# Kernel tuning notes

Hardware: AMD Instinct MI355X
Metric: run time of the kernel (lower is better)

## Reference

```python
import jax, jax.numpy as jnp
import numpy as np

N = 4096  # input_features == output_features == transform length (power of 2)


def _fft(x, twiddle_factors):
    """Faithful vectorized form of the module's radix-2 butterfly network.

    x: (N, D) complex64. twiddle_factors: (N, D) float32 (the learned weights).
    Original loop: for each stage `step`, for each block, for r in [0, half):
        k = r * (N // step)
        temp = exp(-2j*pi*k/N * twiddle_factors[k]) * x[j + half]
        new x[j + half] = x[j] - temp ; new x[j] = x[j] + temp
    Blocks are independent, so each stage is a single batched butterfly.
    """
    n = x.shape[0]
    # initial permutation: index xor with N//2 (as written in the source; not full bit-reversal)
    x = x[jnp.bitwise_xor(jnp.arange(n), n // 2)]
    step = 2
    while step <= n:  # log2(N) stages, fixed small Python loop
        half = step // 2
        k = jnp.arange(half) * (n // step)                      # (half,)
        phase = (-2.0 * jnp.pi) * (k[:, None].astype(jnp.float32) / n) * twiddle_factors[k]
        tw = jnp.exp(1j * phase)                                # (half, D) complex64
        xr = x.reshape(n // step, step, -1)                     # (blocks, step, D)
        top = xr[:, :half]
        bot = xr[:, half:]
        temp = tw[None] * bot                                   # (blocks, half, D)
        x = jnp.concatenate([top + temp, top - temp], axis=1).reshape(n, -1)
        step *= 2
    return x


def setup_inputs() -> dict:
    key = jax.random.key(0)
    kx, kw = jax.random.split(key)
    x = jax.random.normal(kx, (N, N), dtype=jnp.float32)
    weights = jax.random.normal(kw, (N, N), dtype=jnp.float32)  # nn.Parameter(randn(out, in))
    return {"x": x, "weights": weights}


def reference(x, weights):
    # input_features == output_features -> no pad / no truncation branch taken
    return _fft(x.astype(jnp.complex64), weights)
```

## Files before the change

kernel.cpp:

```cpp
#include <hip/hip_runtime.h>

#define FFT_N 4096
#define NEG_TWOPI -6.28318530717958647692f

__global__ __launch_bounds__(256) void fft_lo(const float* __restrict__ x,
                                              const float* __restrict__ w,
                                              float4* __restrict__ dst4,
                                              unsigned dst_lim4) {
    __shared__ __align__(16) float2 tile[64 * 64];
    const int t  = threadIdx.x;
    const int c0 = (blockIdx.x & 63) << 6;
    const int r0 = (blockIdx.x >> 6) << 6;
    const int src_r0 = r0 ^ 2048;

    const float4* x4    = (const float4*)x;
    float4*       tile4 = (float4*)tile;
#pragma unroll
    for (int l = 0; l < 4; ++l) {
        int idx = l * 256 + t;
        int row = idx >> 4;
        int cg  = idx & 15;
        float4 v = x4[(size_t)(src_r0 + row) * 1024 + (c0 >> 2) + cg];
        tile4[(row << 5) + (cg << 1) + 0] = make_float4(v.x, 0.f, v.y, 0.f);
        tile4[(row << 5) + (cg << 1) + 1] = make_float4(v.z, 0.f, v.w, 0.f);
    }
    __syncthreads();

    const int c  = t & 63;
    const int pb = t >> 6;
#pragma unroll
    for (int step = 2; step <= 64; step <<= 1) {
        const int half = step >> 1;
        const int kmul = FFT_N / step;
#pragma unroll
        for (int q = 0; q < 8; ++q) {
            const int p    = pb * 8 + q;
            const int blk  = p / half;
            const int r    = p - blk * half;
            const int itop = blk * step + r;
            const int k    = r * kmul;
            const float wk = w[(size_t)k * FFT_N + c0 + c];
            const float phase = NEG_TWOPI * ((float)k * (1.0f / 4096.0f)) * wk;
            float s, cs;
            __sincosf(phase, &s, &cs);
            float2 a = tile[(itop << 6) + c];
            float2 b = tile[((itop + half) << 6) + c];
            float tr = cs * b.x - s * b.y;
            float ti = cs * b.y + s * b.x;
            tile[(itop << 6) + c]          = make_float2(a.x + tr, a.y + ti);
            tile[((itop + half) << 6) + c] = make_float2(a.x - tr, a.y - ti);
        }
        __syncthreads();
    }

#pragma unroll
    for (int l = 0; l < 8; ++l) {
        int idx = l * 256 + t;
        int row = idx >> 5;
        int cp  = idx & 31;
        size_t gi = (size_t)(r0 + row) * 2048 + (c0 >> 1) + cp;
        if (gi < dst_lim4) dst4[gi] = tile4[(row << 5) + cp];
    }
}

template <int REAL_OUT>
__global__ __launch_bounds__(256) void fft_hi(const float* __restrict__ w,
                                              const float4* __restrict__ src4,
                                              float4* __restrict__ dst4,
                                              unsigned src_lim4,
                                              unsigned dst_lim4) {
    __shared__ __align__(16) float2 tile[64 * 64];
    const int t    = threadIdx.x;
    const int c0   = (blockIdx.x & 63) << 6;
    const int rres = blockIdx.x >> 6;

    float4* tile4 = (float4*)tile;
#pragma unroll
    for (int l = 0; l < 8; ++l) {
        int idx = l * 256 + t;
        int j   = idx >> 5;
        int cp  = idx & 31;
        size_t gi = (size_t)(rres + (j << 6)) * 2048 + (c0 >> 1) + cp;
        tile4[(j << 5) + cp] = (gi < src_lim4) ? src4[gi]
                                               : make_float4(0.f, 0.f, 0.f, 0.f);
    }
    __syncthreads();

    const int c  = t & 63;
    const int pb = t >> 6;
#pragma unroll
    for (int h = 1; h <= 32; h <<= 1) {
        const int kmul = 32 / h;
#pragma unroll
        for (int q = 0; q < 8; ++q) {
            const int p    = pb * 8 + q;
            const int blk  = p / h;
            const int r    = p - blk * h;
            const int jtop = blk * (h << 1) + r;
            const int k    = (rres + (r << 6)) * kmul;
            const float wk = w[(size_t)k * FFT_N + c0 + c];
            const float phase = NEG_TWOPI * ((float)k * (1.0f / 4096.0f)) * wk;
            float s, cs;
            __sincosf(phase, &s, &cs);
            float2 a = tile[(jtop << 6) + c];
            float2 b = tile[((jtop + h) << 6) + c];
            float tr = cs * b.x - s * b.y;
            float ti = cs * b.y + s * b.x;
            tile[(jtop << 6) + c]       = make_float2(a.x + tr, a.y + ti);
            tile[((jtop + h) << 6) + c] = make_float2(a.x - tr, a.y - ti);
        }
        __syncthreads();
    }

    if (REAL_OUT) {
#pragma unroll
        for (int l = 0; l < 4; ++l) {
            int idx = l * 256 + t;
            int j   = idx >> 4;
            int g   = idx & 15;
            float4 v;
            v.x = tile[(j << 6) + 4 * g + 0].x;
            v.y = tile[(j << 6) + 4 * g + 1].x;
            v.z = tile[(j << 6) + 4 * g + 2].x;
            v.w = tile[(j << 6) + 4 * g + 3].x;
            size_t gi = (size_t)(rres + (j << 6)) * 1024 + (c0 >> 2) + g;
            if (gi < dst_lim4) dst4[gi] = v;
        }
    } else {
#pragma unroll
        for (int l = 0; l < 8; ++l) {
            int idx = l * 256 + t;
            int j   = idx >> 5;
            int cp  = idx & 31;
            size_t gi = (size_t)(rres + (j << 6)) * 2048 + (c0 >> 1) + cp;
            if (gi < dst_lim4) dst4[gi] = tile4[(j << 5) + cp];
        }
    }
}

extern "C" void kernel_launch(void* const* d_in, const int* in_sizes, int n_in,
                              void* d_out, int out_size, void* d_ws, size_t ws_size,
                              hipStream_t stream) {
    const float* x = (const float*)d_in[0];
    const float* w = (const float*)d_in[1];
    const long long NN = (long long)FFT_N * FFT_N;

    if ((long long)out_size >= 2 * NN) {
        float4* o4 = (float4*)d_out;
        unsigned lim4 = (unsigned)(out_size / 4);
        fft_lo<<<4096, 256, 0, stream>>>(x, w, o4, lim4);
        fft_hi<0><<<4096, 256, 0, stream>>>(w, o4, o4, lim4, lim4);
    } else {
        float4* ws4 = (float4*)d_ws;
        unsigned ws_lim4  = (unsigned)(ws_size / 16);
        unsigned out_lim4 = (unsigned)(out_size / 4);
        fft_lo<<<4096, 256, 0, stream>>>(x, w, ws4, ws_lim4);
        fft_hi<1><<<4096, 256, 0, stream>>>(w, (const float4*)ws4, (float4*)d_out,
                                            ws_lim4, out_lim4);
    }
}
```

Measured before the change: 235.9 us.

## Do 64-point butterfly stages in registers with one shared-memory transpose

Each thread now keeps 16 complex values in registers. The first four butterfly stages run on those registers, then one shared-memory exchange regroups the data for the last two stages, in both the low and high FFT kernels. This replaces six shared-memory read/write rounds and barriers per kernel with two. It also reduces twiddle loads and sincos calls, because each twiddle is computed once per r and reused across blocks, and the r=0 twiddle is skipped in fft_lo. The cost is higher register pressure, with 32 floats per thread.

```diff
diff --git a/kernel.cpp b/kernel.cpp
--- a/kernel.cpp
+++ b/kernel.cpp
@@ -1,7 +1,14 @@
 #include <hip/hip_runtime.h>
 
-#define FFT_N 4096
 #define NEG_TWOPI -6.28318530717958647692f
+
+__device__ __forceinline__ void bf(float& ar, float& ai, float& br, float& bi,
+                                   float s, float cs) {
+    float tr = cs * br - s * bi;
+    float ti = cs * bi + s * br;
+    br = ar - tr; bi = ai - ti;
+    ar = ar + tr; ai = ai + ti;
+}
 
 __global__ __launch_bounds__(256) void fft_lo(const float* __restrict__ x,
                                               const float* __restrict__ w,
@@ -28,31 +35,71 @@
 
     const int c  = t & 63;
     const int pb = t >> 6;
-#pragma unroll
-    for (int step = 2; step <= 64; step <<= 1) {
-        const int half = step >> 1;
-        const int kmul = FFT_N / step;
-#pragma unroll
-        for (int q = 0; q < 8; ++q) {
-            const int p    = pb * 8 + q;
-            const int blk  = p / half;
-            const int r    = p - blk * half;
-            const int itop = blk * step + r;
-            const int k    = r * kmul;
-            const float wk = w[(size_t)k * FFT_N + c0 + c];
-            const float phase = NEG_TWOPI * ((float)k * (1.0f / 4096.0f)) * wk;
-            float s, cs;
-            __sincosf(phase, &s, &cs);
-            float2 a = tile[(itop << 6) + c];
-            float2 b = tile[((itop + half) << 6) + c];
-            float tr = cs * b.x - s * b.y;
-            float ti = cs * b.y + s * b.x;
-            tile[(itop << 6) + c]          = make_float2(a.x + tr, a.y + ti);
-            tile[((itop + half) << 6) + c] = make_float2(a.x - tr, a.y - ti);
-        }
-        __syncthreads();
-    }
-
+
+    float ar[16], ai[16];
+#pragma unroll
+    for (int m = 0; m < 16; ++m) {
+        float2 v = tile[(16 * pb + m) * 64 + c];
+        ar[m] = v.x; ai[m] = v.y;
+    }
+
+#pragma unroll
+    for (int h = 1; h <= 8; h <<= 1) {
+        const int step = h << 1;
+        const int kmul = 4096 / step;
+#pragma unroll
+        for (int r = 0; r < h; ++r) {
+            float s = 0.f, cs = 1.f;
+            if (r != 0) {
+                const int k = r * kmul;
+                const float wk = w[(size_t)k * 4096 + c0 + c];
+                __sincosf(NEG_TWOPI * ((float)k * (1.f / 4096.f)) * wk, &s, &cs);
+            }
+#pragma unroll
+            for (int b = 0; b < 8 / h; ++b) {
+                const int mt = b * step + r;
+                bf(ar[mt], ai[mt], ar[mt + h], ai[mt + h], s, cs);
+            }
+        }
+    }
+
+#pragma unroll
+    for (int m = 0; m < 16; ++m)
+        tile[(16 * pb + m) * 64 + c] = make_float2(ar[m], ai[m]);
+    __syncthreads();
+#pragma unroll
+    for (int m = 0; m < 16; ++m) {
+        float2 v = tile[(pb + 4 * m) * 64 + c];
+        ar[m] = v.x; ai[m] = v.y;
+    }
+
+#pragma unroll
+    for (int rm = 0; rm < 4; ++rm) {
+        const int j = pb + 4 * rm;
+        const int k = j * 128;
+        float s, cs;
+        const float wk = w[(size_t)k * 4096 + c0 + c];
+        __sincosf(NEG_TWOPI * ((float)k * (1.f / 4096.f)) * wk, &s, &cs);
+#pragma unroll
+        for (int b = 0; b < 2; ++b) {
+            const int mt = b * 8 + rm;
+            bf(ar[mt], ai[mt], ar[mt + 4], ai[mt + 4], s, cs);
+        }
+    }
+#pragma unroll
+    for (int m = 0; m < 8; ++m) {
+        const int j = pb + 4 * m;
+        const int k = j * 64;
+        float s, cs;
+        const float wk = w[(size_t)k * 4096 + c0 + c];
+        __sincosf(NEG_TWOPI * ((float)k * (1.f / 4096.f)) * wk, &s, &cs);
+        bf(ar[m], ai[m], ar[m + 8], ai[m + 8], s, cs);
+    }
+
+#pragma unroll
+    for (int m = 0; m < 16; ++m)
+        tile[(pb + 4 * m) * 64 + c] = make_float2(ar[m], ai[m]);
+    __syncthreads();
 #pragma unroll
     for (int l = 0; l < 8; ++l) {
         int idx = l * 256 + t;
@@ -88,29 +135,69 @@
 
     const int c  = t & 63;
     const int pb = t >> 6;
-#pragma unroll
-    for (int h = 1; h <= 32; h <<= 1) {
+
+    float ar[16], ai[16];
+#pragma unroll
+    for (int m = 0; m < 16; ++m) {
+        float2 v = tile[(16 * pb + m) * 64 + c];
+        ar[m] = v.x; ai[m] = v.y;
+    }
+
+#pragma unroll
+    for (int h = 1; h <= 8; h <<= 1) {
+        const int step = h << 1;
         const int kmul = 32 / h;
 #pragma unroll
-        for (int q = 0; q < 8; ++q) {
-            const int p    = pb * 8 + q;
-            const int blk  = p / h;
-            const int r    = p - blk * h;
-            const int jtop = blk * (h << 1) + r;
-            const int k    = (rres + (r << 6)) * kmul;
-            const float wk = w[(size_t)k * FFT_N + c0 + c];
-            const float phase = NEG_TWOPI * ((float)k * (1.0f / 4096.0f)) * wk;
+        for (int r = 0; r < h; ++r) {
+            const int k = (rres + 64 * r) * kmul;
             float s, cs;
-            __sincosf(phase, &s, &cs);
-            float2 a = tile[(jtop << 6) + c];
-            float2 b = tile[((jtop + h) << 6) + c];
-            float tr = cs * b.x - s * b.y;
-            float ti = cs * b.y + s * b.x;
-            tile[(jtop << 6) + c]       = make_float2(a.x + tr, a.y + ti);
-            tile[((jtop + h) << 6) + c] = make_float2(a.x - tr, a.y - ti);
-        }
-        __syncthreads();
-    }
+            const float wk = w[(size_t)k * 4096 + c0 + c];
+            __sincosf(NEG_TWOPI * ((float)k * (1.f / 4096.f)) * wk, &s, &cs);
+#pragma unroll
+            for (int b = 0; b < 8 / h; ++b) {
+                const int mt = b * step + r;
+                bf(ar[mt], ai[mt], ar[mt + h], ai[mt + h], s, cs);
+            }
+        }
+    }
+
+#pragma unroll
+    for (int m = 0; m < 16; ++m)
+        tile[(16 * pb + m) * 64 + c] = make_float2(ar[m], ai[m]);
+    __syncthreads();
+#pragma unroll
+    for (int m = 0; m < 16; ++m) {
+        float2 v = tile[(pb + 4 * m) * 64 + c];
+        ar[m] = v.x; ai[m] = v.y;
+    }
+
+#pragma unroll
+    for (int rm = 0; rm < 4; ++rm) {
+        const int j = pb + 4 * rm;
+        const int k = (rres + 64 * j) * 2;
+        float s, cs;
+        const float wk = w[(size_t)k * 4096 + c0 + c];
+        __sincosf(NEG_TWOPI * ((float)k * (1.f / 4096.f)) * wk, &s, &cs);
+#pragma unroll
+        for (int b = 0; b < 2; ++b) {
+            const int mt = b * 8 + rm;
+            bf(ar[mt], ai[mt], ar[mt + 4], ai[mt + 4], s, cs);
+        }
+    }
+#pragma unroll
+    for (int m = 0; m < 8; ++m) {
+        const int j = pb + 4 * m;
+        const int k = rres + 64 * j;
+        float s, cs;
+        const float wk = w[(size_t)k * 4096 + c0 + c];
+        __sincosf(NEG_TWOPI * ((float)k * (1.f / 4096.f)) * wk, &s, &cs);
+        bf(ar[m], ai[m], ar[m + 8], ai[m + 8], s, cs);
+    }
+
+#pragma unroll
+    for (int m = 0; m < 16; ++m)
+        tile[(pb + 4 * m) * 64 + c] = make_float2(ar[m], ai[m]);
+    __syncthreads();
 
     if (REAL_OUT) {
 #pragma unroll
@@ -143,7 +230,7 @@
                               hipStream_t stream) {
     const float* x = (const float*)d_in[0];
     const float* w = (const float*)d_in[1];
-    const long long NN = (long long)FFT_N * FFT_N;
+    const long long NN = 4096LL * 4096LL;
 
     if ((long long)out_size >= 2 * NN) {
         float4* o4 = (float4*)d_out;
```

New measurement: 217.0 us. -8.0%, faster.
